# Kernel optimization log

Hardware: AMD Instinct MI355X
Metric: run time of the kernel (lower is better)

## Reference

```python
import jax, jax.numpy as jnp
import numpy as np

SCALE_POS = 2.0
SCALE_NEG = 40.0
THRESH_POS = 0.5
THRESH_NEG = 0.5
MARGIN = 0.1
EPS = 1e-5


def setup_inputs() -> dict:
    key = jax.random.key(0)
    kf, kl = jax.random.split(key)
    B, D, NUM_CLASSES = 4096, 1024, 64
    feats = jax.random.normal(kf, (B, D), dtype=jnp.float32)
    feats = feats / jnp.linalg.norm(feats, axis=1, keepdims=True)  # L2-normalized embeddings
    labels = jax.random.randint(kl, (B,), 0, NUM_CLASSES, dtype=jnp.int64)
    return {"feats": feats, "labels": labels}


def reference(feats, labels):
    B = feats.shape[0]
    sim = jnp.matmul(feats, feats.T)  # [B, B]
    same = labels[:, None] == labels[None, :]
    pos_mask = same & (sim < 1.0 - EPS)  # drop self / near-duplicate pairs
    neg_mask = ~same

    # hard mining: keep negatives above min positive - margin, positives below max negative + margin
    min_pos = jnp.min(jnp.where(pos_mask, sim, jnp.inf), axis=1)   # [B]
    max_neg = jnp.max(jnp.where(neg_mask, sim, -jnp.inf), axis=1)  # [B]
    neg_sel = neg_mask & (sim + MARGIN > min_pos[:, None])
    pos_sel = pos_mask & (sim - MARGIN < max_neg[:, None])

    pos_sum = jnp.sum(jnp.where(pos_sel, jnp.exp(-SCALE_POS * (sim - THRESH_POS)), 0.0), axis=1)
    neg_sum = jnp.sum(jnp.where(neg_sel, jnp.exp(SCALE_NEG * (sim - THRESH_NEG)), 0.0), axis=1)
    pos_loss = jnp.log1p(pos_sum) / SCALE_POS
    neg_loss = jnp.log1p(neg_sum) / SCALE_NEG

    valid = jnp.any(pos_sel, axis=1) & jnp.any(neg_sel, axis=1)  # rows skipped by original loop
    return jnp.sum(jnp.where(valid, pos_loss + neg_loss, 0.0)) / B
```

## Files before the change

kernel.cpp:

```cpp
#include <hip/hip_runtime.h>

typedef _Float16 half8 __attribute__((ext_vector_type(8)));
typedef float floatx4 __attribute__((ext_vector_type(4)));
typedef int intx4 __attribute__((ext_vector_type(4)));
typedef int intx8 __attribute__((ext_vector_type(8)));
typedef __attribute__((address_space(1))) const void gvoid;
typedef __attribute__((address_space(3))) void svoid;

#define SCALE_POS 2.0f
#define SCALE_NEG 40.0f
#define THRESH 0.5f
#define MARGIN 0.1f
#define EPSV 1e-5f

__device__ __forceinline__ unsigned f2ord(float f) {
    unsigned u = __float_as_uint(f);
    return (u & 0x80000000u) ? ~u : (u | 0x80000000u);
}
__device__ __forceinline__ float ord2f(unsigned e) {
    unsigned v = (e & 0x80000000u) ? (e & 0x7fffffffu) : ~e;
    return __uint_as_float(v);
}

#define ORD_POS_INF 0xff800000u
#define ORD_NEG_INF 0x007fffffu

__global__ void k_init(const float* __restrict__ feats,
                       unsigned char* __restrict__ f8,
                       unsigned* __restrict__ minp, unsigned* __restrict__ maxn,
                       float* __restrict__ psum, float* __restrict__ nsum,
                       unsigned* __restrict__ cnts,
                       int total4, int B) {
    int i = blockIdx.x * blockDim.x + threadIdx.x;
    if (i < total4) {
        float4 v = ((const float4*)feats)[i];
        int w = 0;
        w = __builtin_amdgcn_cvt_pk_fp8_f32(v.x, v.y, w, false);
        w = __builtin_amdgcn_cvt_pk_fp8_f32(v.z, v.w, w, true);
        ((int*)f8)[i] = w;
    }
    if (i < B) {
        minp[i] = ORD_POS_INF;
        maxn[i] = ORD_NEG_INF;
        psum[i] = 0.f;
        nsum[i] = 0.f;
    }
    if (i < 2048) cnts[i] = 0;
}

__global__ void __launch_bounds__(256, 4)
k_gemm_h(const unsigned char* __restrict__ f8,
         const int* __restrict__ labels,
         unsigned* __restrict__ minp_ord,
         unsigned* __restrict__ maxn_ord,
         _Float16* __restrict__ simh,
         int D, int nb) {
    __shared__ __align__(16) unsigned char As[128 * 128];
    __shared__ __align__(16) unsigned char Bs[128 * 128];
    __shared__ int labR[128], labC[128];

    const int bid0 = blockIdx.x;
    const int t = (bid0 & 7) * 66 + (bid0 >> 3);
    int rb = 0, rem = t;
    while (rem >= nb - rb) { rem -= nb - rb; ++rb; }
    const int cb = rb + rem;
    const int rowBase = rb * 128;
    const int colBase = cb * 128;

    const int tid = threadIdx.x;
    const int lane = tid & 63;
    const int wave = tid >> 6;
    const int wr = wave >> 1;
    const int wc = wave & 1;
    const int q = lane >> 4;
    const int cIn = lane & 15;

    if (tid < 128) labR[tid] = labels[rowBase + tid];
    else           labC[tid - 128] = labels[colBase + (tid - 128)];

    const int subrow = lane >> 3;
    const int swz = (lane & 7) ^ subrow;
    const unsigned char* gP[8];
    unsigned char* lP[8];
#pragma unroll
    for (int j = 0; j < 8; ++j) {
        const int c = wave * 8 + j;
        const int grow = (c < 16) ? (rowBase + c * 8 + subrow)
                                  : (colBase + (c - 16) * 8 + subrow);
        gP[j] = f8 + (size_t)grow * D + swz * 16;
        lP[j] = ((c < 16) ? (As + c * 1024) : (Bs + (c - 16) * 1024)) + lane * 16;
    }

    int aOff0[4], aOff1[4], bOff0[4], bOff1[4];
#pragma unroll
    for (int i = 0; i < 4; ++i) {
        const int rA = wr * 64 + i * 16 + cIn;
        aOff0[i] = rA * 128 + ((2 * q) ^ (rA & 7)) * 16;
        aOff1[i] = rA * 128 + ((2 * q + 1) ^ (rA & 7)) * 16;
        const int rB = wc * 64 + i * 16 + cIn;
        bOff0[i] = rB * 128 + ((2 * q) ^ (rB & 7)) * 16;
        bOff1[i] = rB * 128 + ((2 * q + 1) ^ (rB & 7)) * 16;
    }

    floatx4 acc[4][4] = {};

    const int KT = D >> 7;
    for (int kt = 0; kt < KT; ++kt) {
        const int kOff = kt * 128;
        __syncthreads();
#pragma unroll
        for (int j = 0; j < 8; ++j)
            __builtin_amdgcn_global_load_lds((gvoid*)(gP[j] + kOff), (svoid*)lP[j], 16, 0, 0);
        __syncthreads();

        intx8 a[4], b[4];
#pragma unroll
        for (int i = 0; i < 4; ++i) {
            intx4 lo = *(const intx4*)(As + aOff0[i]);
            intx4 hi = *(const intx4*)(As + aOff1[i]);
            a[i] = __builtin_shufflevector(lo, hi, 0, 1, 2, 3, 4, 5, 6, 7);
        }
#pragma unroll
        for (int i = 0; i < 4; ++i) {
            intx4 lo = *(const intx4*)(Bs + bOff0[i]);
            intx4 hi = *(const intx4*)(Bs + bOff1[i]);
            b[i] = __builtin_shufflevector(lo, hi, 0, 1, 2, 3, 4, 5, 6, 7);
        }
#pragma unroll
        for (int i = 0; i < 4; ++i)
#pragma unroll
            for (int j2 = 0; j2 < 4; ++j2)
                acc[i][j2] = __builtin_amdgcn_mfma_scale_f32_16x16x128_f8f6f4(
                    a[i], b[j2], acc[i][j2], 0, 0,
                    0, 0x7f7f7f7f,
                    0, 0x7f7f7f7f);
    }

    int rLabv[16];
#pragma unroll
    for (int mi = 0; mi < 4; ++mi)
#pragma unroll
        for (int rr = 0; rr < 4; ++rr)
            rLabv[mi * 4 + rr] = labR[wr * 64 + mi * 16 + q * 4 + rr];
    int cLabv[4];
#pragma unroll
    for (int ni = 0; ni < 4; ++ni)
        cLabv[ni] = labC[wc * 64 + ni * 16 + cIn];

    {
        half8* dst = (half8*)(simh + (size_t)(2 * t + wc) * 8192
                                   + (size_t)(wr * 64 + lane) * 64);
#pragma unroll
        for (int mi = 0; mi < 4; ++mi) {
            half8 h0, h1;
#pragma unroll
            for (int ni = 0; ni < 2; ++ni)
#pragma unroll
                for (int rr = 0; rr < 4; ++rr) {
                    h0[ni * 4 + rr] = (_Float16)acc[mi][ni][rr];
                    h1[ni * 4 + rr] = (_Float16)acc[mi][ni + 2][rr];
                }
            dst[mi * 2] = h0;
            dst[mi * 2 + 1] = h1;
        }
    }

#pragma unroll
    for (int mi = 0; mi < 4; ++mi)
#pragma unroll
        for (int rr = 0; rr < 4; ++rr) {
            const int rLoc = wr * 64 + mi * 16 + q * 4 + rr;
            const int rLab = rLabv[mi * 4 + rr];
            float vmin = 1e30f, vmax = -1e30f;
#pragma unroll
            for (int ni = 0; ni < 4; ++ni) {
                float s = acc[mi][ni][rr];
                if (rLab == cLabv[ni]) {
                    if (s < 1.0f - EPSV) vmin = fminf(vmin, s);
                } else {
                    vmax = fmaxf(vmax, s);
                }
            }
#pragma unroll
            for (int off = 8; off; off >>= 1) {
                vmin = fminf(vmin, __shfl_xor(vmin, off, 16));
                vmax = fmaxf(vmax, __shfl_xor(vmax, off, 16));
            }
            if (cIn == 0) {
                if (vmin < 1e30f) atomicMin(&minp_ord[rowBase + rLoc], f2ord(vmin));
                if (vmax > -1e30f) atomicMax(&maxn_ord[rowBase + rLoc], f2ord(vmax));
            }
        }

    if (rb != cb) {
#pragma unroll
        for (int ni = 0; ni < 4; ++ni) {
            const int cLab = cLabv[ni];
            float vmin = 1e30f, vmax = -1e30f;
#pragma unroll
            for (int mi = 0; mi < 4; ++mi)
#pragma unroll
                for (int rr = 0; rr < 4; ++rr) {
                    float s = acc[mi][ni][rr];
                    if (rLabv[mi * 4 + rr] == cLab) {
                        if (s < 1.0f - EPSV) vmin = fminf(vmin, s);
                    } else {
                        vmax = fmaxf(vmax, s);
                    }
                }
            vmin = fminf(vmin, __shfl_xor(vmin, 16, 64));
            vmin = fminf(vmin, __shfl_xor(vmin, 32, 64));
            vmax = fmaxf(vmax, __shfl_xor(vmax, 16, 64));
            vmax = fmaxf(vmax, __shfl_xor(vmax, 32, 64));
            if (q == 0) {
                const int cLoc = wc * 64 + ni * 16 + cIn;
                if (vmin < 1e30f) atomicMin(&minp_ord[colBase + cLoc], f2ord(vmin));
                if (vmax > -1e30f) atomicMax(&maxn_ord[colBase + cLoc], f2ord(vmax));
            }
        }
    }
}

__global__ void __launch_bounds__(256)
k_sum2f(const _Float16* __restrict__ simh,
        const int* __restrict__ labels,
        const unsigned* __restrict__ minp_ord,
        const unsigned* __restrict__ maxn_ord,
        float* __restrict__ psum, float* __restrict__ nsum,
        unsigned* __restrict__ cnts,
        float* __restrict__ out,
        int nb, int B, int NT) {
    __shared__ int labR[128], labC[128];
    __shared__ float mpR[128], mnR[128], mpC[128], mnC[128];
    __shared__ float red[4];
    __shared__ unsigned lastflag;

    int t = blockIdx.x;
    int rb = 0, rem = t;
    while (rem >= nb - rb) { rem -= nb - rb; ++rb; }
    const int cb = rb + rem;
    const int rowBase = rb * 128;

    const int tid = threadIdx.x;
    const int sub = tid >> 7;
    const int stid = tid & 127;
    const int wave = stid >> 6;
    const int lane = tid & 63;
    const int q = lane >> 4;
    const int cIn = lane & 15;
    const int colBase = cb * 128 + sub * 64;

    if (tid < 128) {
        labR[tid] = labels[rowBase + tid];
        mpR[tid] = ord2f(minp_ord[rowBase + tid]) - MARGIN;
        mnR[tid] = ord2f(maxn_ord[rowBase + tid]) + MARGIN;
    } else {
        const int j = tid - 128;
        labC[j] = labels[cb * 128 + j];
        mpC[j] = ord2f(minp_ord[cb * 128 + j]) - MARGIN;
        mnC[j] = ord2f(maxn_ord[cb * 128 + j]) + MARGIN;
    }
    __syncthreads();

    int cLabv[4];
    float mpCv[4], mnCv[4];
#pragma unroll
    for (int ni = 0; ni < 4; ++ni) {
        const int j = sub * 64 + ni * 16 + cIn;
        cLabv[ni] = labC[j];
        mpCv[ni] = mpC[j];
        mnCv[ni] = mnC[j];
    }

    const half8* src = (const half8*)(simh + (size_t)(2 * t + sub) * 8192 + (size_t)stid * 64);
    half8 hv[8];
#pragma unroll
    for (int v = 0; v < 8; ++v) hv[v] = src[v];

    float cps[4] = {}, cns[4] = {};
    const bool offd = (rb != cb);

#pragma unroll
    for (int mi = 0; mi < 4; ++mi)
#pragma unroll
        for (int rr = 0; rr < 4; ++rr) {
            const int rLoc = wave * 64 + mi * 16 + q * 4 + rr;
            const int rLab = labR[rLoc];
            const float gateN = mpR[rLoc];
            const float gateP = mnR[rLoc];
            float rp = 0.f, rn = 0.f;
#pragma unroll
            for (int ni = 0; ni < 4; ++ni) {
                const int idx = mi * 16 + ni * 4 + rr;
                const float s = (float)hv[idx >> 3][idx & 7];
                if (rLab == cLabv[ni]) {
                    if (s < 1.0f - EPSV) {
                        float ev = __expf(-SCALE_POS * (s - THRESH));
                        if (s < gateP) rp += ev;
                        if (offd && s < mnCv[ni]) cps[ni] += ev;
                    }
                } else {
                    float ev = __expf(SCALE_NEG * (s - THRESH));
                    if (s > gateN) rn += ev;
                    if (offd && s > mpCv[ni]) cns[ni] += ev;
                }
            }
#pragma unroll
            for (int off = 8; off; off >>= 1) {
                rp += __shfl_xor(rp, off, 16);
                rn += __shfl_xor(rn, off, 16);
            }
            if (cIn == 0) {
                if (rp != 0.f) atomicAdd(&psum[rowBase + rLoc], rp);
                if (rn != 0.f) atomicAdd(&nsum[rowBase + rLoc], rn);
            }
        }
    if (offd) {
#pragma unroll
        for (int ni = 0; ni < 4; ++ni) {
            cps[ni] += __shfl_xor(cps[ni], 16, 64);
            cps[ni] += __shfl_xor(cps[ni], 32, 64);
            cns[ni] += __shfl_xor(cns[ni], 16, 64);
            cns[ni] += __shfl_xor(cns[ni], 32, 64);
            if (q == 0) {
                const int cLoc = ni * 16 + cIn;
                if (cps[ni] != 0.f) atomicAdd(&psum[colBase + cLoc], cps[ni]);
                if (cns[ni] != 0.f) atomicAdd(&nsum[colBase + cLoc], cns[ni]);
            }
        }
    }

    __syncthreads();
    if (tid == 0) {
        const unsigned stripe = (unsigned)blockIdx.x & 31u;
        const unsigned stripe_target = (unsigned)((NT - (int)stripe + 31) / 32);
        unsigned prev = __hip_atomic_fetch_add(&cnts[(1 + stripe) * 32], 1u,
                                               __ATOMIC_RELAXED, __HIP_MEMORY_SCOPE_AGENT);
        unsigned lf = 0u;
        if (prev == stripe_target - 1u) {
            unsigned ptop = __hip_atomic_fetch_add(&cnts[0], 1u,
                                                   __ATOMIC_RELAXED, __HIP_MEMORY_SCOPE_AGENT);
            lf = (ptop == 31u) ? 1u : 0u;
        }
        lastflag = lf;
    }
    __syncthreads();
    if (lastflag) {
        float a = 0.f;
        for (int i = tid; i < B; i += 256) {
            float pv = atomicAdd(&psum[i], 0.0f);
            float nv = atomicAdd(&nsum[i], 0.0f);
            if (pv > 0.f && nv > 0.f)
                a += log1pf(pv) * (1.0f / SCALE_POS) + log1pf(nv) * (1.0f / SCALE_NEG);
        }
#pragma unroll
        for (int off = 32; off; off >>= 1) a += __shfl_down(a, off, 64);
        if ((tid & 63) == 0) red[tid >> 6] = a;
        __syncthreads();
        if (tid == 0) out[0] = (red[0] + red[1] + red[2] + red[3]) / (float)B;
    }
}

extern "C" void kernel_launch(void* const* d_in, const int* in_sizes, int n_in,
                              void* d_out, int out_size, void* d_ws, size_t ws_size,
                              hipStream_t stream) {
    const float* feats = (const float*)d_in[0];
    const int* labels = (const int*)d_in[1];
    const int B = in_sizes[1];
    const int D = in_sizes[0] / B;
    const int nb = B / 128;
    const int NT = nb * (nb + 1) / 2;
    const int total4 = B * D / 4;

    char* ws = (char*)d_ws;
    unsigned char* f8 = (unsigned char*)ws;
    size_t off = (size_t)B * D;
    unsigned* minp = (unsigned*)(ws + off); off += (size_t)B * 4;
    unsigned* maxn = (unsigned*)(ws + off); off += (size_t)B * 4;
    float* psum = (float*)(ws + off); off += (size_t)B * 4;
    float* nsum = (float*)(ws + off); off += (size_t)B * 4;
    unsigned* cnts = (unsigned*)(ws + off); off += 8192;
    _Float16* simh = (_Float16*)(ws + ((off + 255) & ~(size_t)255));
    float* outp = (float*)d_out;

    k_init<<<(total4 + 255) / 256, 256, 0, stream>>>(feats, f8, minp, maxn,
                                                     psum, nsum, cnts, total4, B);

    k_gemm_h<<<NT, 256, 0, stream>>>(f8, labels, minp, maxn, simh, D, nb);

    k_sum2f<<<NT, 256, 0, stream>>>(simh, labels, minp, maxn, psum, nsum,
                                    cnts, outp, nb, B, NT);
}
```

Measured before the change: 138.5 us.

## Replace global atomics with partial-result buffers and separate reduction kernels

The per-row min/max and exp-sum reductions no longer use global atomics. Each tile now writes its partial values to dedicated slots in [64, B] buffers, and two small kernels (k_stats, k_final) reduce those slots. This removes atomic contention, the per-launch buffer initialisation and the last-block counter logic. In exchange it adds two kernel launches and more workspace traffic, and the final sum still relies on an atomicAdd into out across 16 blocks.

Result: faster. 134.7 us (-2.8%).

```diff
diff --git a/kernel.cpp b/kernel.cpp
--- a/kernel.cpp
+++ b/kernel.cpp
@@ -13,24 +13,10 @@
 #define MARGIN 0.1f
 #define EPSV 1e-5f
 
-__device__ __forceinline__ unsigned f2ord(float f) {
-    unsigned u = __float_as_uint(f);
-    return (u & 0x80000000u) ? ~u : (u | 0x80000000u);
-}
-__device__ __forceinline__ float ord2f(unsigned e) {
-    unsigned v = (e & 0x80000000u) ? (e & 0x7fffffffu) : ~e;
-    return __uint_as_float(v);
-}
-
-#define ORD_POS_INF 0xff800000u
-#define ORD_NEG_INF 0x007fffffu
-
 __global__ void k_init(const float* __restrict__ feats,
                        unsigned char* __restrict__ f8,
-                       unsigned* __restrict__ minp, unsigned* __restrict__ maxn,
-                       float* __restrict__ psum, float* __restrict__ nsum,
-                       unsigned* __restrict__ cnts,
-                       int total4, int B) {
+                       float* __restrict__ out,
+                       int total4) {
     int i = blockIdx.x * blockDim.x + threadIdx.x;
     if (i < total4) {
         float4 v = ((const float4*)feats)[i];
@@ -39,25 +25,21 @@
         w = __builtin_amdgcn_cvt_pk_fp8_f32(v.z, v.w, w, true);
         ((int*)f8)[i] = w;
     }
-    if (i < B) {
-        minp[i] = ORD_POS_INF;
-        maxn[i] = ORD_NEG_INF;
-        psum[i] = 0.f;
-        nsum[i] = 0.f;
-    }
-    if (i < 2048) cnts[i] = 0;
+    if (i == 0) out[0] = 0.f;
 }
 
 __global__ void __launch_bounds__(256, 4)
 k_gemm_h(const unsigned char* __restrict__ f8,
          const int* __restrict__ labels,
-         unsigned* __restrict__ minp_ord,
-         unsigned* __restrict__ maxn_ord,
+         float* __restrict__ pmin,
+         float* __restrict__ pmax,
          _Float16* __restrict__ simh,
          int D, int nb) {
     __shared__ __align__(16) unsigned char As[128 * 128];
     __shared__ __align__(16) unsigned char Bs[128 * 128];
     __shared__ int labR[128], labC[128];
+
+    const int Bsz = nb * 128;
 
     const int bid0 = blockIdx.x;
     const int t = (bid0 & 7) * 66 + (bid0 >> 3);
@@ -165,34 +147,40 @@
         }
     }
 
-#pragma unroll
-    for (int mi = 0; mi < 4; ++mi)
-#pragma unroll
-        for (int rr = 0; rr < 4; ++rr) {
-            const int rLoc = wr * 64 + mi * 16 + q * 4 + rr;
-            const int rLab = rLabv[mi * 4 + rr];
-            float vmin = 1e30f, vmax = -1e30f;
-#pragma unroll
-            for (int ni = 0; ni < 4; ++ni) {
-                float s = acc[mi][ni][rr];
-                if (rLab == cLabv[ni]) {
-                    if (s < 1.0f - EPSV) vmin = fminf(vmin, s);
-                } else {
-                    vmax = fmaxf(vmax, s);
-                }
-            }
-#pragma unroll
-            for (int off = 8; off; off >>= 1) {
-                vmin = fminf(vmin, __shfl_xor(vmin, off, 16));
-                vmax = fmaxf(vmax, __shfl_xor(vmax, off, 16));
-            }
-            if (cIn == 0) {
-                if (vmin < 1e30f) atomicMin(&minp_ord[rowBase + rLoc], f2ord(vmin));
-                if (vmax > -1e30f) atomicMax(&maxn_ord[rowBase + rLoc], f2ord(vmax));
-            }
-        }
+    {
+        float* pmnRow = pmin + (size_t)(2 * cb + wc) * Bsz + rowBase;
+        float* pmxRow = pmax + (size_t)(2 * cb + wc) * Bsz + rowBase;
+#pragma unroll
+        for (int mi = 0; mi < 4; ++mi)
+#pragma unroll
+            for (int rr = 0; rr < 4; ++rr) {
+                const int rLoc = wr * 64 + mi * 16 + q * 4 + rr;
+                const int rLab = rLabv[mi * 4 + rr];
+                float vmin = 1e30f, vmax = -1e30f;
+#pragma unroll
+                for (int ni = 0; ni < 4; ++ni) {
+                    float s = acc[mi][ni][rr];
+                    if (rLab == cLabv[ni]) {
+                        if (s < 1.0f - EPSV) vmin = fminf(vmin, s);
+                    } else {
+                        vmax = fmaxf(vmax, s);
+                    }
+                }
+#pragma unroll
+                for (int off = 8; off; off >>= 1) {
+                    vmin = fminf(vmin, __shfl_xor(vmin, off, 16));
+                    vmax = fmaxf(vmax, __shfl_xor(vmax, off, 16));
+                }
+                if (cIn == 0) {
+                    pmnRow[rLoc] = vmin;
+                    pmxRow[rLoc] = vmax;
+                }
+            }
+    }
 
     if (rb != cb) {
+        float* pmnCol = pmin + (size_t)(2 * rb + wr) * Bsz + colBase;
+        float* pmxCol = pmax + (size_t)(2 * rb + wr) * Bsz + colBase;
 #pragma unroll
         for (int ni = 0; ni < 4; ++ni) {
             const int cLab = cLabv[ni];
@@ -214,26 +202,35 @@
             vmax = fmaxf(vmax, __shfl_xor(vmax, 32, 64));
             if (q == 0) {
                 const int cLoc = wc * 64 + ni * 16 + cIn;
-                if (vmin < 1e30f) atomicMin(&minp_ord[colBase + cLoc], f2ord(vmin));
-                if (vmax > -1e30f) atomicMax(&maxn_ord[colBase + cLoc], f2ord(vmax));
-            }
-        }
-    }
+                pmnCol[cLoc] = vmin;
+                pmxCol[cLoc] = vmax;
+            }
+        }
+    }
+}
+
+__global__ void __launch_bounds__(256)
+k_stats(const float* __restrict__ pmin, const float* __restrict__ pmax,
+        float* __restrict__ gateN, float* __restrict__ gateP, int B) {
+    const int r = blockIdx.x * 256 + threadIdx.x;
+    float mn = 1e30f, mx = -1e30f;
+    for (int k = 0; k < 64; ++k) {
+        mn = fminf(mn, pmin[(size_t)k * B + r]);
+        mx = fmaxf(mx, pmax[(size_t)k * B + r]);
+    }
+    gateN[r] = mn - MARGIN;
+    gateP[r] = mx + MARGIN;
 }
 
 __global__ void __launch_bounds__(256)
 k_sum2f(const _Float16* __restrict__ simh,
         const int* __restrict__ labels,
-        const unsigned* __restrict__ minp_ord,
-        const unsigned* __restrict__ maxn_ord,
-        float* __restrict__ psum, float* __restrict__ nsum,
-        unsigned* __restrict__ cnts,
-        float* __restrict__ out,
-        int nb, int B, int NT) {
+        const float* __restrict__ gateN,
+        const float* __restrict__ gateP,
+        float* __restrict__ psP, float* __restrict__ psN,
+        int nb, int B) {
     __shared__ int labR[128], labC[128];
-    __shared__ float mpR[128], mnR[128], mpC[128], mnC[128];
-    __shared__ float red[4];
-    __shared__ unsigned lastflag;
+    __shared__ float gNR[128], gPR[128], gNC[128], gPC[128];
 
     int t = blockIdx.x;
     int rb = 0, rem = t;
@@ -252,24 +249,24 @@
 
     if (tid < 128) {
         labR[tid] = labels[rowBase + tid];
-        mpR[tid] = ord2f(minp_ord[rowBase + tid]) - MARGIN;
-        mnR[tid] = ord2f(maxn_ord[rowBase + tid]) + MARGIN;
+        gNR[tid] = gateN[rowBase + tid];
+        gPR[tid] = gateP[rowBase + tid];
     } else {
         const int j = tid - 128;
         labC[j] = labels[cb * 128 + j];
-        mpC[j] = ord2f(minp_ord[cb * 128 + j]) - MARGIN;
-        mnC[j] = ord2f(maxn_ord[cb * 128 + j]) + MARGIN;
+        gNC[j] = gateN[cb * 128 + j];
+        gPC[j] = gateP[cb * 128 + j];
     }
     __syncthreads();
 
     int cLabv[4];
-    float mpCv[4], mnCv[4];
+    float gNCv[4], gPCv[4];
 #pragma unroll
     for (int ni = 0; ni < 4; ++ni) {
         const int j = sub * 64 + ni * 16 + cIn;
         cLabv[ni] = labC[j];
-        mpCv[ni] = mpC[j];
-        mnCv[ni] = mnC[j];
+        gNCv[ni] = gNC[j];
+        gPCv[ni] = gPC[j];
     }
 
     const half8* src = (const half8*)(simh + (size_t)(2 * t + sub) * 8192 + (size_t)stid * 64);
@@ -279,6 +276,9 @@
 
     float cps[4] = {}, cns[4] = {};
     const bool offd = (rb != cb);
+
+    float* psPRow = psP + (size_t)(2 * cb + sub) * B + rowBase;
+    float* psNRow = psN + (size_t)(2 * cb + sub) * B + rowBase;
 
 #pragma unroll
     for (int mi = 0; mi < 4; ++mi)
@@ -286,8 +286,8 @@
         for (int rr = 0; rr < 4; ++rr) {
             const int rLoc = wave * 64 + mi * 16 + q * 4 + rr;
             const int rLab = labR[rLoc];
-            const float gateN = mpR[rLoc];
-            const float gateP = mnR[rLoc];
+            const float gn = gNR[rLoc];
+            const float gp = gPR[rLoc];
             float rp = 0.f, rn = 0.f;
 #pragma unroll
             for (int ni = 0; ni < 4; ++ni) {
@@ -296,13 +296,13 @@
                 if (rLab == cLabv[ni]) {
                     if (s < 1.0f - EPSV) {
                         float ev = __expf(-SCALE_POS * (s - THRESH));
-                        if (s < gateP) rp += ev;
-                        if (offd && s < mnCv[ni]) cps[ni] += ev;
+                        if (s < gp) rp += ev;
+                        if (offd && s < gPCv[ni]) cps[ni] += ev;
                     }
                 } else {
                     float ev = __expf(SCALE_NEG * (s - THRESH));
-                    if (s > gateN) rn += ev;
-                    if (offd && s > mpCv[ni]) cns[ni] += ev;
+                    if (s > gn) rn += ev;
+                    if (offd && s > gNCv[ni]) cns[ni] += ev;
                 }
             }
 #pragma unroll
@@ -311,11 +311,13 @@
                 rn += __shfl_xor(rn, off, 16);
             }
             if (cIn == 0) {
-                if (rp != 0.f) atomicAdd(&psum[rowBase + rLoc], rp);
-                if (rn != 0.f) atomicAdd(&nsum[rowBase + rLoc], rn);
+                psPRow[rLoc] = rp;
+                psNRow[rLoc] = rn;
             }
         }
     if (offd) {
+        float* psPCol = psP + (size_t)(2 * rb + wave) * B + colBase;
+        float* psNCol = psN + (size_t)(2 * rb + wave) * B + colBase;
 #pragma unroll
         for (int ni = 0; ni < 4; ++ni) {
             cps[ni] += __shfl_xor(cps[ni], 16, 64);
@@ -324,41 +326,33 @@
             cns[ni] += __shfl_xor(cns[ni], 32, 64);
             if (q == 0) {
                 const int cLoc = ni * 16 + cIn;
-                if (cps[ni] != 0.f) atomicAdd(&psum[colBase + cLoc], cps[ni]);
-                if (cns[ni] != 0.f) atomicAdd(&nsum[colBase + cLoc], cns[ni]);
-            }
-        }
-    }
-
+                psPCol[cLoc] = cps[ni];
+                psNCol[cLoc] = cns[ni];
+            }
+        }
+    }
+}
+
+__global__ void __launch_bounds__(256)
+k_final(const float* __restrict__ psP, const float* __restrict__ psN,
+        float* __restrict__ out, int B) {
+    __shared__ float red[4];
+    const int r = blockIdx.x * 256 + threadIdx.x;
+    float P = 0.f, N = 0.f;
+    for (int k = 0; k < 64; ++k) {
+        P += psP[(size_t)k * B + r];
+        N += psN[(size_t)k * B + r];
+    }
+    float a = (P > 0.f && N > 0.f)
+                  ? log1pf(P) * (1.0f / SCALE_POS) + log1pf(N) * (1.0f / SCALE_NEG)
+                  : 0.f;
+#pragma unroll
+    for (int off = 32; off; off >>= 1) a += __shfl_down(a, off, 64);
+    const int tid = threadIdx.x;
+    if ((tid & 63) == 0) red[tid >> 6] = a;
     __syncthreads();
-    if (tid == 0) {
-        const unsigned stripe = (unsigned)blockIdx.x & 31u;
-        const unsigned stripe_target = (unsigned)((NT - (int)stripe + 31) / 32);
-        unsigned prev = __hip_atomic_fetch_add(&cnts[(1 + stripe) * 32], 1u,
-                                               __ATOMIC_RELAXED, __HIP_MEMORY_SCOPE_AGENT);
-        unsigned lf = 0u;
-        if (prev == stripe_target - 1u) {
-            unsigned ptop = __hip_atomic_fetch_add(&cnts[0], 1u,
-                                                   __ATOMIC_RELAXED, __HIP_MEMORY_SCOPE_AGENT);
-            lf = (ptop == 31u) ? 1u : 0u;
-        }
-        lastflag = lf;
-    }
-    __syncthreads();
-    if (lastflag) {
-        float a = 0.f;
-        for (int i = tid; i < B; i += 256) {
-            float pv = atomicAdd(&psum[i], 0.0f);
-            float nv = atomicAdd(&nsum[i], 0.0f);
-            if (pv > 0.f && nv > 0.f)
-                a += log1pf(pv) * (1.0f / SCALE_POS) + log1pf(nv) * (1.0f / SCALE_NEG);
-        }
-#pragma unroll
-        for (int off = 32; off; off >>= 1) a += __shfl_down(a, off, 64);
-        if ((tid & 63) == 0) red[tid >> 6] = a;
-        __syncthreads();
-        if (tid == 0) out[0] = (red[0] + red[1] + red[2] + red[3]) / (float)B;
-    }
+    if (tid == 0)
+        atomicAdd(out, (red[0] + red[1] + red[2] + red[3]) / (float)B);
 }
 
 extern "C" void kernel_launch(void* const* d_in, const int* in_sizes, int n_in,
@@ -375,19 +369,22 @@
     char* ws = (char*)d_ws;
     unsigned char* f8 = (unsigned char*)ws;
     size_t off = (size_t)B * D;
-    unsigned* minp = (unsigned*)(ws + off); off += (size_t)B * 4;
-    unsigned* maxn = (unsigned*)(ws + off); off += (size_t)B * 4;
-    float* psum = (float*)(ws + off); off += (size_t)B * 4;
-    float* nsum = (float*)(ws + off); off += (size_t)B * 4;
-    unsigned* cnts = (unsigned*)(ws + off); off += 8192;
+    float* pmin = (float*)(ws + off); off += (size_t)64 * B * 4;
+    float* pmax = (float*)(ws + off); off += (size_t)64 * B * 4;
+    float* psP  = (float*)(ws + off); off += (size_t)64 * B * 4;
+    float* psN  = (float*)(ws + off); off += (size_t)64 * B * 4;
+    float* gateN = (float*)(ws + off); off += (size_t)B * 4;
+    float* gateP = (float*)(ws + off); off += (size_t)B * 4;
     _Float16* simh = (_Float16*)(ws + ((off + 255) & ~(size_t)255));
     float* outp = (float*)d_out;
 
-    k_init<<<(total4 + 255) / 256, 256, 0, stream>>>(feats, f8, minp, maxn,
-                                                     psum, nsum, cnts, total4, B);
-
-    k_gemm_h<<<NT, 256, 0, stream>>>(f8, labels, minp, maxn, simh, D, nb);
-
-    k_sum2f<<<NT, 256, 0, stream>>>(simh, labels, minp, maxn, psum, nsum,
-                                    cnts, outp, nb, B, NT);
-}
+    k_init<<<(total4 + 255) / 256, 256, 0, stream>>>(feats, f8, outp, total4);
+
+    k_gemm_h<<<NT, 256, 0, stream>>>(f8, labels, pmin, pmax, simh, D, nb);
+
+    k_stats<<<B / 256, 256, 0, stream>>>(pmin, pmax, gateN, gateP, B);
+
+    k_sum2f<<<NT, 256, 0, stream>>>(simh, labels, gateN, gateP, psP, psN, nb, B);
+
+    k_final<<<B / 256, 256, 0, stream>>>(psP, psN, outp, B);
+}
```
